# Optimization experiments

Hardware: AMD Instinct MI355X
Metric: run time of the kernel (lower is better)

## Reference

```python
import jax, jax.numpy as jnp
import numpy as np

T = 64      # simulation_length
B = 128     # batch
D = 2048    # flattened input dim / axons per core
N = 2048    # neurons per core
L = 4       # number of cores (chain, latency = index)
OUT = 1024  # number of output_sources


def setup_inputs() -> dict:
    key = jax.random.key(0)
    k0, k1, k2, k3 = jax.random.split(key, 4)
    x = jax.random.uniform(k0, (B, D), dtype=jnp.float32)          # rate-coded input in [0,1)
    # core_params[l] = core_matrix.transpose() -> shape [N, A]; scaled for sane membrane dynamics
    W = jax.random.normal(k1, (L, N, D), dtype=jnp.float32) * 0.05
    thresholds = jnp.ones((L,), dtype=jnp.float32)
    # axon_sources: per-core irregular gather indices into previous core's neurons (input for l=0)
    axon_idx = jax.random.randint(k2, (L, D), 0, D, dtype=jnp.int32)
    out_idx = jax.random.randint(k3, (OUT,), 0, N, dtype=jnp.int32)
    return dict(x=x, W=W, thresholds=thresholds, axon_idx=axon_idx,
                out_idx=out_idx, simulation_length=T)


def _ideal_spike_scan(avg, thr, T):
    """Per-cycle: m += avg; spike = (m > thr); m[m > thr] -= thr.  avg: [B, N]."""
    def step(m, _):
        m = m + avg
        s = (m > thr).astype(m.dtype)
        return m - thr * s, s
    _, spikes = jax.lax.scan(step, jnp.zeros_like(avg), None, length=T)
    return spikes  # [T, B, N]


def reference(x, W, thresholds, axon_idx, out_idx, simulation_length):
    T = simulation_length
    L = W.shape[0]
    # generate_input_spike_train: x replicated across all cycles -> cache[-1]
    prev = jnp.broadcast_to(x, (T,) + x.shape)  # [T, B, D]
    for l in range(L):
        # get_signal_tensor: gather axon source signals for every cycle
        gathered = prev[:, :, axon_idx[l]]                    # [T, B, A]
        # per-cycle matmul: torch.matmul(core_params, sig.T).T == sig @ W[l].T
        val = jnp.einsum('tba,na->tbn', gathered, W[l])       # [T, B, N]
        avg = val.mean(axis=0)                                # avg_values [B, N]
        # ideal membrane integrate + threshold-reset recurrence -> out spike train
        prev = _ideal_spike_scan(avg, thresholds[l], T)       # [T, B, N]
    # output_signals: sum of output-source spikes over all cycles
    return prev[:, :, out_idx].sum(axis=0)                    # [B, OUT]
```

## Files before the change

kernel.cpp:

```cpp
#include <hip/hip_runtime.h>

#define BB   128
#define DD   2048
#define NN   2048
#define LL   4
#define OUTN 1024
#define JBW  64

typedef double double4v __attribute__((ext_vector_type(4)));

__global__ __launch_bounds__(256) void gather0_kernel(
    const float* __restrict__ x, const int* __restrict__ idx0,
    float* __restrict__ At)
{
    int i = blockIdx.x * 256 + threadIdx.x;
    int k = i >> 7;
    int b = i & 127;
    At[i] = x[b * DD + idx0[k]];
}

__global__ __launch_bounds__(128, 2) void layer_kernel(
    const float* __restrict__ srcT,
    const int*   __restrict__ idx,
    const float* __restrict__ Wl,
    const float* __restrict__ thresholds, int l,
    const int*   __restrict__ Tptr,
    float* __restrict__ dst, int isLast)
{
    __shared__ double red[256];

    const int t    = threadIdx.x;
    const int wk   = t >> 6;
    const int lane = t & 63;
    const int q    = lane >> 4;
    const int c    = lane & 15;

    const int g     = blockIdx.x;
    const int ntile = g & 127;
    const int btile = g >> 7;
    const int n0    = ntile * 16;
    const int bcol  = btile * 16 + c;

    double4v pr = {0., 0., 0., 0.}, pcv = {0., 0., 0., 0.};
    pr  = __builtin_amdgcn_mfma_f64_16x16x4f64(0.25 * (double)c, 1.0, pr, 0, 0, 0);
    pcv = __builtin_amdgcn_mfma_f64_16x16x4f64(0.25, (double)c, pcv, 0, 0, 0);
    int rowD[4], colD[4];
    #pragma unroll
    for (int r = 0; r < 4; ++r) {
        rowD[r] = (int)(pr[r] + 0.25);
        colD[r] = (int)(pcv[r] + 0.25);
    }

    double4v acc[4] = {{0.,0.,0.,0.},{0.,0.,0.,0.},{0.,0.,0.,0.},{0.,0.,0.,0.}};

    const int    kbase = wk * (DD / 2);
    const float* wbase = Wl + (size_t)(n0 + c) * DD + kbase + 4 * q;
    const int*   ibase = idx ? (idx + kbase + 4 * q) : nullptr;

    float4 wv[4];
    int4   iv[4];
    float4 sv[4];

    #pragma unroll
    for (int p = 0; p < 4; ++p) wv[p] = *(const float4*)(wbase + 16 * p);
    #pragma unroll
    for (int p = 0; p < 4; ++p) {
        int r0, r1, r2, r3;
        if (ibase) {
            int4 iv0 = *(const int4*)(ibase + 16 * p);
            r0 = iv0.x; r1 = iv0.y; r2 = iv0.z; r3 = iv0.w;
        } else {
            int kb = kbase + 16 * p + 4 * q;
            r0 = kb; r1 = kb + 1; r2 = kb + 2; r3 = kb + 3;
        }
        sv[p].x = srcT[(size_t)r0 * BB + bcol];
        sv[p].y = srcT[(size_t)r1 * BB + bcol];
        sv[p].z = srcT[(size_t)r2 * BB + bcol];
        sv[p].w = srcT[(size_t)r3 * BB + bcol];
    }
    if (ibase) {
        #pragma unroll
        for (int p = 0; p < 4; ++p) iv[p] = *(const int4*)(ibase + 16 * (4 + p));
    }

    for (int u = 0; u < JBW / 4; ++u) {
        #pragma unroll
        for (int gg = 0; gg < 4; ++gg) {
            float4 wcur = wv[gg];
            float4 scur = sv[gg];

            int jn = 4 * u + 4 + gg; if (jn > JBW - 1) jn = JBW - 1;
            wv[gg] = *(const float4*)(wbase + 16 * jn);

            int r0, r1, r2, r3;
            if (ibase) {
                int4 ivv = iv[gg];
                r0 = ivv.x; r1 = ivv.y; r2 = ivv.z; r3 = ivv.w;
            } else {
                int kb = kbase + 16 * jn + 4 * q;
                r0 = kb; r1 = kb + 1; r2 = kb + 2; r3 = kb + 3;
            }
            sv[gg].x = srcT[(size_t)r0 * BB + bcol];
            sv[gg].y = srcT[(size_t)r1 * BB + bcol];
            sv[gg].z = srcT[(size_t)r2 * BB + bcol];
            sv[gg].w = srcT[(size_t)r3 * BB + bcol];

            if (ibase) {
                int jm = 4 * u + 8 + gg; if (jm > JBW - 1) jm = JBW - 1;
                iv[gg] = *(const int4*)(ibase + 16 * jm);
            }

            acc[0] = __builtin_amdgcn_mfma_f64_16x16x4f64((double)wcur.x, (double)scur.x, acc[0], 0, 0, 0);
            acc[1] = __builtin_amdgcn_mfma_f64_16x16x4f64((double)wcur.y, (double)scur.y, acc[1], 0, 0, 0);
            acc[2] = __builtin_amdgcn_mfma_f64_16x16x4f64((double)wcur.z, (double)scur.z, acc[2], 0, 0, 0);
            acc[3] = __builtin_amdgcn_mfma_f64_16x16x4f64((double)wcur.w, (double)scur.w, acc[3], 0, 0, 0);
        }
    }

    double4v a = (acc[0] + acc[1]) + (acc[2] + acc[3]);

    if (wk == 1) {
        #pragma unroll
        for (int r = 0; r < 4; ++r) red[lane * 4 + r] = a[r];
    }
    __syncthreads();
    if (wk == 0) {
        #pragma unroll
        for (int r = 0; r < 4; ++r) a[r] += red[lane * 4 + r];

        const double th = (double)thresholds[l];
        const int T = *Tptr;
        const float sc = isLast ? 1.0f : (1.0f / (float)T);
        double m0 = 0., m1 = 0., m2 = 0., m3 = 0.;
        int c0 = 0, c1 = 0, c2 = 0, c3 = 0;
        for (int tt = 0; tt < T; ++tt) {
            m0 += a[0]; if (m0 > th) { c0++; m0 -= th; }
            m1 += a[1]; if (m1 > th) { c1++; m1 -= th; }
            m2 += a[2]; if (m2 > th) { c2++; m2 -= th; }
            m3 += a[3]; if (m3 > th) { c3++; m3 -= th; }
        }
        int cnt[4] = {c0, c1, c2, c3};
        #pragma unroll
        for (int r = 0; r < 4; ++r) {
            int n = n0 + rowD[r];
            dst[(size_t)n * BB + btile * 16 + colD[r]] = (float)cnt[r] * sc;
        }
    }
}

__global__ __launch_bounds__(256) void out_kernel(
    const float* __restrict__ cntT, const int* __restrict__ out_idx,
    float* __restrict__ out)
{
    int i = blockIdx.x * 256 + threadIdx.x;
    int b = i >> 10;
    int o = i & 1023;
    out[i] = cntT[(size_t)out_idx[o] * BB + b];
}

extern "C" void kernel_launch(void* const* d_in, const int* in_sizes, int n_in,
                              void* d_out, int out_size, void* d_ws, size_t ws_size,
                              hipStream_t stream)
{
    const float* x    = (const float*)d_in[0];
    const float* W    = (const float*)d_in[1];
    const float* thr  = (const float*)d_in[2];
    const int*   axon = (const int*)d_in[3];
    const int*   oidx = (const int*)d_in[4];
    const int*   Tptr = (const int*)d_in[5];
    float* out = (float*)d_out;

    char* ws = (char*)d_ws;
    float* At   = (float*)ws;
    float* mA   = (float*)(ws + (1u << 20));
    float* mB   = (float*)(ws + (2u << 20));
    float* cntT = (float*)(ws + (3u << 20));

    gather0_kernel<<<(DD * BB) / 256, 256, 0, stream>>>(x, axon, At);

    const float* srcs[LL] = { At, mA, mB, mA };
    float*       dsts[LL] = { mA, mB, mA, cntT };
    for (int l = 0; l < LL; ++l) {
        const int* idx = (l == 0) ? nullptr : (axon + (size_t)l * DD);
        layer_kernel<<<1024, 128, 0, stream>>>(
            srcs[l], idx, W + (size_t)l * NN * DD, thr, l, Tptr,
            dsts[l], (l == LL - 1) ? 1 : 0);
    }

    out_kernel<<<(BB * OUTN) / 256, 256, 0, stream>>>(cntT, oidx, out);
}
```

Measured before the change: 241.0 us.

## Widen layer tile to 32 neurons and split K across four waves

Each block now computes a 32-neuron by 16-batch tile with 256 threads, and the K dimension is split across four waves instead of two. Each gathered source value is reused for two neuron sub-tiles, which halves the irregular gather traffic per MFMA. Block ids are remapped so that neighbouring blocks share neuron super-tiles across batch tiles, which should improve L2 reuse of W. The cost is higher register pressure from doubled accumulators and weight buffers, plus a four-way LDS reduction.

```diff
diff --git a/kernel.cpp b/kernel.cpp
--- a/kernel.cpp
+++ b/kernel.cpp
@@ -5,7 +5,7 @@
 #define NN   2048
 #define LL   4
 #define OUTN 1024
-#define JBW  64
+#define JBQ  32
 
 typedef double double4v __attribute__((ext_vector_type(4)));
 
@@ -19,7 +19,7 @@
     At[i] = x[b * DD + idx0[k]];
 }
 
-__global__ __launch_bounds__(128, 2) void layer_kernel(
+__global__ __launch_bounds__(256, 2) void layer_kernel(
     const float* __restrict__ srcT,
     const int*   __restrict__ idx,
     const float* __restrict__ Wl,
@@ -27,18 +27,18 @@
     const int*   __restrict__ Tptr,
     float* __restrict__ dst, int isLast)
 {
-    __shared__ double red[256];
+    __shared__ double red[4 * 64 * 8];
 
     const int t    = threadIdx.x;
-    const int wk   = t >> 6;
+    const int wq   = t >> 6;
     const int lane = t & 63;
     const int q    = lane >> 4;
     const int c    = lane & 15;
 
     const int g     = blockIdx.x;
-    const int ntile = g & 127;
-    const int btile = g >> 7;
-    const int n0    = ntile * 16;
+    const int btile = (g >> 3) & 7;
+    const int nsup  = (g & 7) | ((g >> 6) << 3);
+    const int n0    = nsup * 32;
     const int bcol  = btile * 16 + c;
 
     double4v pr = {0., 0., 0., 0.}, pcv = {0., 0., 0., 0.};
@@ -51,18 +51,23 @@
         colD[r] = (int)(pcv[r] + 0.25);
     }
 
-    double4v acc[4] = {{0.,0.,0.,0.},{0.,0.,0.,0.},{0.,0.,0.,0.},{0.,0.,0.,0.}};
-
-    const int    kbase = wk * (DD / 2);
-    const float* wbase = Wl + (size_t)(n0 + c) * DD + kbase + 4 * q;
+    double4v acc0[4] = {{0.,0.,0.,0.},{0.,0.,0.,0.},{0.,0.,0.,0.},{0.,0.,0.,0.}};
+    double4v acc1[4] = {{0.,0.,0.,0.},{0.,0.,0.,0.},{0.,0.,0.,0.},{0.,0.,0.,0.}};
+
+    const int    kbase = wq * (DD / 4);
+    const float* wb0   = Wl + (size_t)(n0 + c) * DD + kbase + 4 * q;
+    const float* wb1   = wb0 + (size_t)16 * DD;
     const int*   ibase = idx ? (idx + kbase + 4 * q) : nullptr;
 
-    float4 wv[4];
+    float4 wv0[4], wv1[4];
+    float4 sv[4];
     int4   iv[4];
-    float4 sv[4];
 
     #pragma unroll
-    for (int p = 0; p < 4; ++p) wv[p] = *(const float4*)(wbase + 16 * p);
+    for (int p = 0; p < 4; ++p) {
+        wv0[p] = *(const float4*)(wb0 + 16 * p);
+        wv1[p] = *(const float4*)(wb1 + 16 * p);
+    }
     #pragma unroll
     for (int p = 0; p < 4; ++p) {
         int r0, r1, r2, r3;
@@ -83,14 +88,16 @@
         for (int p = 0; p < 4; ++p) iv[p] = *(const int4*)(ibase + 16 * (4 + p));
     }
 
-    for (int u = 0; u < JBW / 4; ++u) {
+    for (int u = 0; u < JBQ / 4; ++u) {
         #pragma unroll
         for (int gg = 0; gg < 4; ++gg) {
-            float4 wcur = wv[gg];
-            float4 scur = sv[gg];
-
-            int jn = 4 * u + 4 + gg; if (jn > JBW - 1) jn = JBW - 1;
-            wv[gg] = *(const float4*)(wbase + 16 * jn);
+            float4 w0 = wv0[gg];
+            float4 w1 = wv1[gg];
+            float4 s  = sv[gg];
+
+            int jn = 4 * u + 4 + gg; if (jn > JBQ - 1) jn = JBQ - 1;
+            wv0[gg] = *(const float4*)(wb0 + 16 * jn);
+            wv1[gg] = *(const float4*)(wb1 + 16 * jn);
 
             int r0, r1, r2, r3;
             if (ibase) {
@@ -106,27 +113,40 @@
             sv[gg].w = srcT[(size_t)r3 * BB + bcol];
 
             if (ibase) {
-                int jm = 4 * u + 8 + gg; if (jm > JBW - 1) jm = JBW - 1;
+                int jm = 4 * u + 8 + gg; if (jm > JBQ - 1) jm = JBQ - 1;
                 iv[gg] = *(const int4*)(ibase + 16 * jm);
             }
 
-            acc[0] = __builtin_amdgcn_mfma_f64_16x16x4f64((double)wcur.x, (double)scur.x, acc[0], 0, 0, 0);
-            acc[1] = __builtin_amdgcn_mfma_f64_16x16x4f64((double)wcur.y, (double)scur.y, acc[1], 0, 0, 0);
-            acc[2] = __builtin_amdgcn_mfma_f64_16x16x4f64((double)wcur.z, (double)scur.z, acc[2], 0, 0, 0);
-            acc[3] = __builtin_amdgcn_mfma_f64_16x16x4f64((double)wcur.w, (double)scur.w, acc[3], 0, 0, 0);
-        }
-    }
-
-    double4v a = (acc[0] + acc[1]) + (acc[2] + acc[3]);
-
-    if (wk == 1) {
-        #pragma unroll
-        for (int r = 0; r < 4; ++r) red[lane * 4 + r] = a[r];
+            acc0[0] = __builtin_amdgcn_mfma_f64_16x16x4f64((double)w0.x, (double)s.x, acc0[0], 0, 0, 0);
+            acc1[0] = __builtin_amdgcn_mfma_f64_16x16x4f64((double)w1.x, (double)s.x, acc1[0], 0, 0, 0);
+            acc0[1] = __builtin_amdgcn_mfma_f64_16x16x4f64((double)w0.y, (double)s.y, acc0[1], 0, 0, 0);
+            acc1[1] = __builtin_amdgcn_mfma_f64_16x16x4f64((double)w1.y, (double)s.y, acc1[1], 0, 0, 0);
+            acc0[2] = __builtin_amdgcn_mfma_f64_16x16x4f64((double)w0.z, (double)s.z, acc0[2], 0, 0, 0);
+            acc1[2] = __builtin_amdgcn_mfma_f64_16x16x4f64((double)w1.z, (double)s.z, acc1[2], 0, 0, 0);
+            acc0[3] = __builtin_amdgcn_mfma_f64_16x16x4f64((double)w0.w, (double)s.w, acc0[3], 0, 0, 0);
+            acc1[3] = __builtin_amdgcn_mfma_f64_16x16x4f64((double)w1.w, (double)s.w, acc1[3], 0, 0, 0);
+        }
+    }
+
+    double4v a0 = (acc0[0] + acc0[1]) + (acc0[2] + acc0[3]);
+    double4v a1 = (acc1[0] + acc1[1]) + (acc1[2] + acc1[3]);
+
+    {
+        double* my = red + ((size_t)wq * 64 + lane) * 8;
+        #pragma unroll
+        for (int r = 0; r < 4; ++r) { my[r] = a0[r]; my[4 + r] = a1[r]; }
     }
     __syncthreads();
-    if (wk == 0) {
-        #pragma unroll
-        for (int r = 0; r < 4; ++r) a[r] += red[lane * 4 + r];
+    if (wq < 2) {
+        const int off = wq * 4;
+        double a[4];
+        #pragma unroll
+        for (int r = 0; r < 4; ++r) {
+            a[r] =  red[((size_t)0 * 64 + lane) * 8 + off + r];
+            a[r] += red[((size_t)1 * 64 + lane) * 8 + off + r];
+            a[r] += red[((size_t)2 * 64 + lane) * 8 + off + r];
+            a[r] += red[((size_t)3 * 64 + lane) * 8 + off + r];
+        }
 
         const double th = (double)thresholds[l];
         const int T = *Tptr;
@@ -142,7 +162,7 @@
         int cnt[4] = {c0, c1, c2, c3};
         #pragma unroll
         for (int r = 0; r < 4; ++r) {
-            int n = n0 + rowD[r];
+            int n = n0 + 16 * wq + rowD[r];
             dst[(size_t)n * BB + btile * 16 + colD[r]] = (float)cnt[r] * sc;
         }
     }
@@ -182,7 +202,7 @@
     float*       dsts[LL] = { mA, mB, mA, cntT };
     for (int l = 0; l < LL; ++l) {
         const int* idx = (l == 0) ? nullptr : (axon + (size_t)l * DD);
-        layer_kernel<<<1024, 128, 0, stream>>>(
+        layer_kernel<<<512, 256, 0, stream>>>(
             srcs[l], idx, W + (size_t)l * NN * DD, thr, l, Tptr,
             dsts[l], (l == LL - 1) ? 1 : 0);
     }
```

Measured after the change: 227.6 us. 5.6% less time.
